# Kernel tuning notes

Measured on AMD Instinct MI355X. Metric: run time of the kernel, lower is better.

Reference implementation:

```python
import jax, jax.numpy as jnp
import numpy as np

THRESHOLD = 0.7
STRIDE = 1
PADDING = 1


def setup_inputs() -> dict:
    key = jax.random.key(0)
    k1, k2 = jax.random.split(key)
    B, CIN, H, W = 32, 256, 56, 56
    COUT, K = 256, 3
    x = jax.random.normal(k1, (B, CIN, H, W), dtype=jnp.float32)
    # kaiming-uniform-ish init: U(-bound, bound), bound = sqrt(6/fan_in)
    fan_in = CIN * K * K
    bound = float(np.sqrt(6.0 / fan_in))
    weight = jax.random.uniform(k2, (COUT, CIN, K, K), dtype=jnp.float32,
                                minval=-bound, maxval=bound)
    alpha = jnp.ones((1,), dtype=jnp.float32)
    bias = jnp.zeros((COUT,), dtype=jnp.float32)
    return {"x": x, "weight": weight, "alpha": alpha, "bias": bias}


def _ternize_ste(w, threshold):
    delta = threshold * jnp.mean(jnp.abs(jax.lax.stop_gradient(w)))
    ternary = jnp.where(w > delta, 1.0,
                        jnp.where(w < -delta, -1.0, 0.0)).astype(w.dtype)
    # straight-through: value = ternary, gradient = identity w.r.t. w
    return ternary + (w - jax.lax.stop_gradient(w))


def reference(x, weight, alpha, bias):
    w_t = _ternize_ste(weight, THRESHOLD) * alpha  # [COUT, CIN, K, K]
    out = jax.lax.conv_general_dilated(
        x, w_t,
        window_strides=(STRIDE, STRIDE),
        padding=[(PADDING, PADDING), (PADDING, PADDING)],
        dimension_numbers=("NCHW", "OIHW", "NCHW"),
    )
    return out + bias[None, :, None, None]
```

## Files before the change

### kernel.cpp

```cpp
#include <hip/hip_runtime.h>

typedef unsigned short ushort_t;
typedef short short8 __attribute__((ext_vector_type(8)));
typedef unsigned short ushort8 __attribute__((ext_vector_type(8)));
typedef float floatx4 __attribute__((ext_vector_type(4)));

#define N_W 589824

static __device__ __forceinline__ unsigned short f2bf(float f) {
    unsigned int u = __float_as_uint(f);
    u = (u + 0x7FFFu + ((u >> 16) & 1u)) >> 16;
    return (unsigned short)u;
}

static __device__ __forceinline__ void g2l16(const void* g, void* lds_base_uniform) {
    __builtin_amdgcn_global_load_lds(
        (__attribute__((address_space(1))) void*)g,
        (__attribute__((address_space(3))) void*)lds_base_uniform,
        16, 0, 0);
}

__global__ void absmean_kernel(const float* __restrict__ w, double* __restrict__ dsum) {
    int tid = blockIdx.x * blockDim.x + threadIdx.x;
    int stride = gridDim.x * blockDim.x;
    float local = 0.f;
    for (int i = tid; i < N_W; i += stride) local += fabsf(w[i]);
    for (int off = 32; off > 0; off >>= 1)
        local += __shfl_down(local, off, 64);
    __shared__ float part[4];
    int lane = threadIdx.x & 63, wv = threadIdx.x >> 6;
    if (lane == 0) part[wv] = local;
    __syncthreads();
    if (threadIdx.x == 0) {
        float s = part[0] + part[1] + part[2] + part[3];
        atomicAdd(dsum, (double)s);
    }
}

__global__ void ternarize_frag_kernel(const float* __restrict__ w, const double* __restrict__ dsum,
                                      ushort_t* __restrict__ wtf) {
    int o = blockIdx.x * 256 + threadIdx.x;
    float delta = 0.7f * (float)(*dsum / (double)N_W);
    int e   = o & 7;
    int l   = (o >> 3) & 15;
    int q   = (o >> 7) & 3;
    int i   = (o >> 9) & 3;
    int g   = (o >> 11) & 3;
    int t13 = o >> 13;
    int r9  = t13 % 9;
    int cb  = t13 / 9;
    int co  = g * 64 + i * 16 + l;
    int cin = cb * 32 + q * 8 + e;
    float v = w[(co * 256 + cin) * 9 + r9];
    float t = (v > delta) ? 1.f : ((v < -delta) ? -1.f : 0.f);
    wtf[o] = f2bf(t);
}

__global__ void ternarize_kernel(const float* __restrict__ w, const double* __restrict__ dsum,
                                 ushort_t* __restrict__ wt) {
    int o = blockIdx.x * 256 + threadIdx.x;
    float delta = 0.7f * (float)(*dsum / (double)N_W);
    int cin = o & 255;
    int co  = (o >> 8) & 255;
    int r   = o >> 16;
    float v = w[(co * 256 + cin) * 9 + r];
    float t = (v > delta) ? 1.f : ((v < -delta) ? -1.f : 0.f);
    wt[o] = f2bf(t);
}

__global__ void border_zero_kernel(ushort_t* __restrict__ xp) {
    int e = blockIdx.x * 256 + threadIdx.x;
    int cg   = e & 31;
    int rest = e >> 5;
    int pid  = rest % 228;
    int b    = rest / 228;
    int hh, ww;
    if (pid < 58)       { hh = 0;  ww = pid; }
    else if (pid < 116) { hh = 57; ww = pid - 58; }
    else {
        int p = pid - 116;
        hh = 1 + (p >> 1);
        ww = (p & 1) ? 57 : 0;
    }
    ushort8 z = (ushort8){0,0,0,0,0,0,0,0};
    *(ushort8*)&xp[(((b * 58 + hh) * 58 + ww) << 8) + cg * 8] = z;
}

__global__ __launch_bounds__(256)
void xcvt_kernel(const float* __restrict__ x, ushort_t* __restrict__ xp) {
    __shared__ float tile[64][65];
    const int px0 = blockIdx.x * 64;
    const int ci0 = blockIdx.y * 64;
    const int b   = blockIdx.z;
    const int row  = threadIdx.x >> 6;
    const int lane = threadIdx.x & 63;
#pragma unroll
    for (int k = 0; k < 16; ++k) {
        int ci_l = row * 16 + k;
        tile[ci_l][lane] = x[(b * 256 + ci0 + ci_l) * 3136 + px0 + lane];
    }
    __syncthreads();
#pragma unroll
    for (int p = 0; p < 2; ++p) {
        int c    = threadIdx.x + p * 256;
        int px_l = c >> 3;
        int cg   = c & 7;
        int px = px0 + px_l;
        int h = px / 56, w = px - h * 56;
        ushort8 v;
#pragma unroll
        for (int j = 0; j < 8; ++j) v[j] = f2bf(tile[cg * 8 + j][px_l]);
        *(ushort8*)&xp[(((b * 58 + h + 1) * 58 + (w + 1)) << 8) + ci0 + cg * 8] = v;
    }
}

__global__ __launch_bounds__(256, 3)
void conv_mfma4_kernel(const ushort_t* __restrict__ xp, const ushort_t* __restrict__ wtf,
                       const float* __restrict__ alpha, const float* __restrict__ bias,
                       float* __restrict__ out) {
    __shared__ __align__(16) ushort_t lds_x[2 * 512 * 8];

    const int tid  = threadIdx.x;
    const int b    = blockIdx.y;
    const int th   = blockIdx.x / 7;
    const int tw   = blockIdx.x - th * 7;
    const int h0   = th * 8;
    const int w0   = tw * 8;

    const int lane = tid & 63;
    const int wave = tid >> 6;
    const int l15  = lane & 15;
    const int quad = lane >> 4;
    const int hs   = l15 >> 3;
    const int ws   = l15 & 7;

    unsigned goff[2], loff[2];
#pragma unroll
    for (int t = 0; t < 2; ++t) {
        int s  = tid + t * 256;
        int ss = (s < 400) ? s : 399;
        int hr  = ss / 40;
        int rem = ss - hr * 40;
        int wc  = rem >> 2, cig = rem & 3;
        int gh = h0 + hr;
        int gw = w0 + wc;
        goff[t] = (unsigned)(((((b * 58 + gh) * 58 + gw) << 8) + (cig << 3)) * 2);
        loff[t] = (unsigned)((s & ~63) * 16);
    }
    const char* xpb = (const char*)xp;

    floatx4 acc[4][4];
#pragma unroll
    for (int i = 0; i < 4; ++i)
#pragma unroll
        for (int j = 0; j < 4; ++j)
            acc[i][j] = (floatx4){0.f, 0.f, 0.f, 0.f};

    const int gsel = wave;
    const ushort_t* wbase = wtf + gsel * 2048 + lane * 8;

    short8 af[3][4];
#pragma unroll
    for (int r = 0; r < 3; ++r)
#pragma unroll
        for (int i = 0; i < 4; ++i)
            af[r][i] = *(const short8*)(wbase + r * 8192 + i * 512);

#pragma unroll
    for (int t = 0; t < 2; ++t)
        g2l16(xpb + goff[t], (char*)lds_x + loff[t]);

    const int baseB = (hs * 10 + ws) * 32 + quad * 8;

    int cur = 0;
    for (int cb = 0; cb < 8; ++cb) {
        const ushort_t* wcb = wbase + cb * 73728;
        const ushort_t* wnx = wbase + ((cb < 7) ? cb + 1 : cb) * 73728;

        __syncthreads();

        if (cb < 7) {
#pragma unroll
            for (int t = 0; t < 2; ++t)
                g2l16(xpb + goff[t] + (cb + 1) * 64, (char*)lds_x + loff[t] + (cur ^ 1) * 8192);
        }

        const ushort_t* xb = lds_x + cur * 4096;

        short8 bfv[2][4];
#pragma unroll
        for (int j = 0; j < 4; ++j)
            bfv[0][j] = *(const short8*)&xb[baseB + (j * 2) * 320];

#pragma unroll
        for (int r9 = 0; r9 < 9; ++r9) {
            if (r9 < 8) {
                const int kh1 = (r9 + 1) / 3;
                const int kw1 = (r9 + 1) - kh1 * 3;
#pragma unroll
                for (int j = 0; j < 4; ++j)
                    bfv[(r9 + 1) & 1][j] =
                        *(const short8*)&xb[baseB + ((j * 2 + kh1) * 10 + kw1) * 32];
            }
            __builtin_amdgcn_s_setprio(1);
#pragma unroll
            for (int i = 0; i < 4; ++i)
#pragma unroll
                for (int j = 0; j < 4; ++j)
                    acc[i][j] = __builtin_amdgcn_mfma_f32_16x16x32_bf16(
                        af[r9 % 3][i], bfv[r9 & 1][j], acc[i][j], 0, 0, 0);
            __builtin_amdgcn_s_setprio(0);
            {
                const ushort_t* asrc = (r9 < 6) ? (wcb + (r9 + 3) * 8192)
                                                : (wnx + (r9 - 6) * 8192);
#pragma unroll
                for (int i = 0; i < 4; ++i)
                    af[r9 % 3][i] = *(const short8*)(asrc + i * 512);
            }
        }
        cur ^= 1;
    }

    const float a0 = alpha[0];
#pragma unroll
    for (int i = 0; i < 4; ++i) {
        int cob = gsel * 64 + i * 16 + quad * 4;
#pragma unroll
        for (int j = 0; j < 4; ++j) {
            int hh = h0 + j * 2 + hs;
            int ww = w0 + ws;
#pragma unroll
            for (int r = 0; r < 4; ++r) {
                int cog = cob + r;
                out[((b * 256 + cog) * 56 + hh) * 56 + ww] = acc[i][j][r] * a0 + bias[cog];
            }
        }
    }
}

__global__ __launch_bounds__(256, 2)
void conv_mfma_fallback_kernel(const float* __restrict__ x, const ushort_t* __restrict__ wt,
                               const float* __restrict__ alpha, const float* __restrict__ bias,
                               float* __restrict__ out) {
    __shared__ __align__(16) ushort_t lds_x[10 * 18 * 40];
    __shared__ __align__(16) ushort_t lds_a[128 * 40];
    const int tid  = threadIdx.x;
    const int b    = blockIdx.y;
    const int th   = blockIdx.x >> 2;
    const int tw   = blockIdx.x & 3;
    const int h0   = th * 8;
    const int w0   = tw * 16;
    const int co0  = blockIdx.z * 128;
    const int lane = tid & 63;
    const int wave = tid >> 6;
    const int l15  = lane & 15;
    const int quad = lane >> 4;
    const int wco  = (wave & 1) * 64;
    const int wrow = (wave >> 1) * 4;
    floatx4 acc[4][4];
#pragma unroll
    for (int i = 0; i < 4; ++i)
#pragma unroll
        for (int j = 0; j < 4; ++j)
            acc[i][j] = (floatx4){0.f, 0.f, 0.f, 0.f};
    const int co_l = tid >> 1;
    const int half = tid & 1;
    for (int cin0 = 0; cin0 < 256; cin0 += 32) {
        for (int e = tid; e < 5760; e += 256) {
            int hc = e % 18;
            int t2 = e / 18;
            int hr = t2 % 10;
            int ci = t2 / 10;
            int hh = h0 - 1 + hr;
            int ww = w0 - 1 + hc;
            float v = 0.f;
            if (hh >= 0 && hh < 56 && ww >= 0 && ww < 56)
                v = x[((b * 256 + cin0 + ci) * 3136) + hh * 56 + ww];
            lds_x[(hr * 18 + hc) * 40 + ci] = f2bf(v);
        }
        for (int r9 = 0; r9 < 9; ++r9) {
            {
                const short8* src = (const short8*)(wt + (((r9 * 256) + co0 + co_l) * 256 + cin0 + half * 16));
                short8 v0 = src[0];
                short8 v1 = src[1];
                *(short8*)&lds_a[co_l * 40 + half * 16]     = v0;
                *(short8*)&lds_a[co_l * 40 + half * 16 + 8] = v1;
            }
            __syncthreads();
            const int kh = r9 / 3;
            const int kw = r9 % 3;
            short8 af[4], bf[4];
#pragma unroll
            for (int j = 0; j < 4; ++j)
                bf[j] = *(const short8*)&lds_x[((wrow + j + kh) * 18 + (l15 + kw)) * 40 + quad * 8];
#pragma unroll
            for (int i = 0; i < 4; ++i)
                af[i] = *(const short8*)&lds_a[(wco + i * 16 + l15) * 40 + quad * 8];
#pragma unroll
            for (int i = 0; i < 4; ++i)
#pragma unroll
                for (int j = 0; j < 4; ++j)
                    acc[i][j] = __builtin_amdgcn_mfma_f32_16x16x32_bf16(af[i], bf[j], acc[i][j], 0, 0, 0);
            __syncthreads();
        }
    }
    const float a0 = alpha[0];
#pragma unroll
    for (int i = 0; i < 4; ++i) {
        int cob = co0 + wco + i * 16 + quad * 4;
#pragma unroll
        for (int j = 0; j < 4; ++j) {
            int hh = h0 + wrow + j;
            int ww = w0 + l15;
            if (ww < 56) {
#pragma unroll
                for (int r = 0; r < 4; ++r) {
                    int cog = cob + r;
                    out[((b * 256 + cog) * 56 + hh) * 56 + ww] = acc[i][j][r] * a0 + bias[cog];
                }
            }
        }
    }
}

extern "C" void kernel_launch(void* const* d_in, const int* in_sizes, int n_in,
                              void* d_out, int out_size, void* d_ws, size_t ws_size,
                              hipStream_t stream) {
    const float* x      = (const float*)d_in[0];
    const float* weight = (const float*)d_in[1];
    const float* alpha  = (const float*)d_in[2];
    const float* bias   = (const float*)d_in[3];
    float* out = (float*)d_out;

    double*   dsum = (double*)d_ws;
    ushort_t* wtf  = (ushort_t*)((char*)d_ws + 256);
    ushort_t* xp   = (ushort_t*)((char*)d_ws + 256 + 1179648);
    const size_t NEED = 256 + 1179648 + 55115776;

    hipMemsetAsync(d_ws, 0, 16, stream);
    absmean_kernel<<<256, 256, 0, stream>>>(weight, dsum);

    if (ws_size >= NEED) {
        ternarize_frag_kernel<<<N_W / 256, 256, 0, stream>>>(weight, dsum, wtf);
        border_zero_kernel<<<912, 256, 0, stream>>>(xp);
        dim3 cgrid(49, 4, 32);
        xcvt_kernel<<<cgrid, 256, 0, stream>>>(x, xp);
        dim3 grid(49, 32);
        conv_mfma4_kernel<<<grid, 256, 0, stream>>>(xp, wtf, alpha, bias, out);
    } else {
        ternarize_kernel<<<N_W / 256, 256, 0, stream>>>(weight, dsum, wtf);
        dim3 grid(28, 32, 2);
        conv_mfma_fallback_kernel<<<grid, 256, 0, stream>>>(x, wtf, alpha, bias, out);
    }
}
```

Baseline: 337.7 us.

## Store ternary weights as int8 bytes, expand to bf16 in-register; merge prep kernels

Ternary weights are now stored as one byte per element, holding the high byte of bf16 ±1/0, and expanded to bf16 with v_perm right before each MFMA. This halves the weight fragment traffic in the conv loop. The ternarize, border-zero and x-convert kernels are merged into a single prep launch that uses extra grid columns, which removes two launches. The block-level __syncthreads is replaced with an explicit waitcnt plus barrier, so the prefetched weight loads can stay in flight. The cost is some extra VALU perm work per r9 step and reliance on a hand-tuned vmcnt that has to match the number of outstanding loads.

```diff
diff --git a/kernel.cpp b/kernel.cpp
--- a/kernel.cpp
+++ b/kernel.cpp
@@ -1,9 +1,12 @@
 #include <hip/hip_runtime.h>
 
 typedef unsigned short ushort_t;
+typedef unsigned char uchar_t;
 typedef short short8 __attribute__((ext_vector_type(8)));
 typedef unsigned short ushort8 __attribute__((ext_vector_type(8)));
 typedef float floatx4 __attribute__((ext_vector_type(4)));
+typedef unsigned int uint2v __attribute__((ext_vector_type(2)));
+typedef unsigned int uint4v __attribute__((ext_vector_type(4)));
 
 #define N_W 589824
 
@@ -18,6 +21,15 @@
         (__attribute__((address_space(1))) void*)g,
         (__attribute__((address_space(3))) void*)lds_base_uniform,
         16, 0, 0);
+}
+
+static __device__ __forceinline__ short8 expand_tern(uint2v c) {
+    uint4v r;
+    r[0] = __builtin_amdgcn_perm(0x80808080u, c[0], 0x01040004u);
+    r[1] = __builtin_amdgcn_perm(0x80808080u, c[0], 0x03040204u);
+    r[2] = __builtin_amdgcn_perm(0x80808080u, c[1], 0x01040004u);
+    r[3] = __builtin_amdgcn_perm(0x80808080u, c[1], 0x03040204u);
+    return __builtin_bit_cast(short8, r);
 }
 
 __global__ void absmean_kernel(const float* __restrict__ w, double* __restrict__ dsum) {
@@ -37,23 +49,79 @@
     }
 }
 
-__global__ void ternarize_frag_kernel(const float* __restrict__ w, const double* __restrict__ dsum,
-                                      ushort_t* __restrict__ wtf) {
-    int o = blockIdx.x * 256 + threadIdx.x;
-    float delta = 0.7f * (float)(*dsum / (double)N_W);
-    int e   = o & 7;
-    int l   = (o >> 3) & 15;
-    int q   = (o >> 7) & 3;
-    int i   = (o >> 9) & 3;
-    int g   = (o >> 11) & 3;
-    int t13 = o >> 13;
-    int r9  = t13 % 9;
-    int cb  = t13 / 9;
-    int co  = g * 64 + i * 16 + l;
-    int cin = cb * 32 + q * 8 + e;
-    float v = w[(co * 256 + cin) * 9 + r9];
-    float t = (v > delta) ? 1.f : ((v < -delta) ? -1.f : 0.f);
-    wtf[o] = f2bf(t);
+__global__ __launch_bounds__(256)
+void prep_kernel(const float* __restrict__ x, const float* __restrict__ w,
+                 const double* __restrict__ dsum,
+                 uchar_t* __restrict__ wtf, ushort_t* __restrict__ xp) {
+    const int tid = threadIdx.x;
+
+    if (blockIdx.x == 50) {
+        const int id = blockIdx.y * 32 + blockIdx.z;
+        const float delta = 0.7f * (float)(*dsum / (double)N_W);
+        for (int k = tid; k < 4608; k += 256) {
+            int o = id * 4608 + k;
+            int e   = o & 7;
+            int l   = (o >> 3) & 15;
+            int q   = (o >> 7) & 3;
+            int i   = (o >> 9) & 3;
+            int g   = (o >> 11) & 3;
+            int t13 = o >> 13;
+            int r9  = t13 % 9;
+            int cb  = t13 / 9;
+            int co  = g * 64 + i * 16 + l;
+            int cin = cb * 32 + q * 8 + e;
+            float v = w[(co * 256 + cin) * 9 + r9];
+            wtf[o] = (v > delta) ? 0x3F : ((v < -delta) ? 0xBF : 0x00);
+        }
+        return;
+    }
+
+    if (blockIdx.x == 49) {
+        const int id = blockIdx.y * 32 + blockIdx.z;
+        ushort8 z = (ushort8){0,0,0,0,0,0,0,0};
+        for (int k = tid; k < 1824; k += 256) {
+            int e = id * 1824 + k;
+            int cg   = e & 31;
+            int rest = e >> 5;
+            int pid  = rest % 228;
+            int b    = rest / 228;
+            int hh, ww;
+            if (pid < 58)       { hh = 0;  ww = pid; }
+            else if (pid < 116) { hh = 57; ww = pid - 58; }
+            else {
+                int p = pid - 116;
+                hh = 1 + (p >> 1);
+                ww = (p & 1) ? 57 : 0;
+            }
+            *(ushort8*)&xp[(((b * 58 + hh) * 58 + ww) << 8) + cg * 8] = z;
+        }
+        return;
+    }
+
+    __shared__ float tile[64][65];
+    const int px0 = blockIdx.x * 64;
+    const int ci0 = blockIdx.y * 64;
+    const int b   = blockIdx.z;
+    const int row  = tid >> 6;
+    const int lane = tid & 63;
+#pragma unroll
+    for (int k = 0; k < 16; ++k) {
+        int ci_l = row * 16 + k;
+        tile[ci_l][lane] = x[(b * 256 + ci0 + ci_l) * 3136 + px0 + lane];
+    }
+    __syncthreads();
+#pragma unroll
+    for (int p = 0; p < 2; ++p) {
+        int c    = tid + p * 256;
+        int px_l = c >> 3;
+        int cg   = c & 7;
+        int px = px0 + px_l;
+        int h = px / 56, w2 = px - h * 56;
+        ushort8 v;
+#pragma unroll
+        for (int j = 0; j < 8; ++j) v[j] = f2bf(tile[cg * 8 + j][px_l]);
+        *(ushort8*)&xp[(((b * 58 + h + 1) * 58 + (w2 + 1)) << 8) + ci0 + cg * 8] = v;
+    }
 }
 
 __global__ void ternarize_kernel(const float* __restrict__ w, const double* __restrict__ dsum,
@@ -68,54 +136,8 @@
     wt[o] = f2bf(t);
 }
 
-__global__ void border_zero_kernel(ushort_t* __restrict__ xp) {
-    int e = blockIdx.x * 256 + threadIdx.x;
-    int cg   = e & 31;
-    int rest = e >> 5;
-    int pid  = rest % 228;
-    int b    = rest / 228;
-    int hh, ww;
-    if (pid < 58)       { hh = 0;  ww = pid; }
-    else if (pid < 116) { hh = 57; ww = pid - 58; }
-    else {
-        int p = pid - 116;
-        hh = 1 + (p >> 1);
-        ww = (p & 1) ? 57 : 0;
-    }
-    ushort8 z = (ushort8){0,0,0,0,0,0,0,0};
-    *(ushort8*)&xp[(((b * 58 + hh) * 58 + ww) << 8) + cg * 8] = z;
-}
-
-__global__ __launch_bounds__(256)
-void xcvt_kernel(const float* __restrict__ x, ushort_t* __restrict__ xp) {
-    __shared__ float tile[64][65];
-    const int px0 = blockIdx.x * 64;
-    const int ci0 = blockIdx.y * 64;
-    const int b   = blockIdx.z;
-    const int row  = threadIdx.x >> 6;
-    const int lane = threadIdx.x & 63;
-#pragma unroll
-    for (int k = 0; k < 16; ++k) {
-        int ci_l = row * 16 + k;
-        tile[ci_l][lane] = x[(b * 256 + ci0 + ci_l) * 3136 + px0 + lane];
-    }
-    __syncthreads();
-#pragma unroll
-    for (int p = 0; p < 2; ++p) {
-        int c    = threadIdx.x + p * 256;
-        int px_l = c >> 3;
-        int cg   = c & 7;
-        int px = px0 + px_l;
-        int h = px / 56, w = px - h * 56;
-        ushort8 v;
-#pragma unroll
-        for (int j = 0; j < 8; ++j) v[j] = f2bf(tile[cg * 8 + j][px_l]);
-        *(ushort8*)&xp[(((b * 58 + h + 1) * 58 + (w + 1)) << 8) + ci0 + cg * 8] = v;
-    }
-}
-
 __global__ __launch_bounds__(256, 3)
-void conv_mfma4_kernel(const ushort_t* __restrict__ xp, const ushort_t* __restrict__ wtf,
+void conv_mfma5_kernel(const ushort_t* __restrict__ xp, const uchar_t* __restrict__ wtf,
                        const float* __restrict__ alpha, const float* __restrict__ bias,
                        float* __restrict__ out) {
     __shared__ __align__(16) ushort_t lds_x[2 * 512 * 8];
@@ -157,33 +179,36 @@
             acc[i][j] = (floatx4){0.f, 0.f, 0.f, 0.f};
 
     const int gsel = wave;
-    const ushort_t* wbase = wtf + gsel * 2048 + lane * 8;
-
-    short8 af[3][4];
-#pragma unroll
-    for (int r = 0; r < 3; ++r)
-#pragma unroll
-        for (int i = 0; i < 4; ++i)
-            af[r][i] = *(const short8*)(wbase + r * 8192 + i * 512);
+    const uchar_t* wbase = wtf + gsel * 2048 + lane * 8;
 
 #pragma unroll
     for (int t = 0; t < 2; ++t)
         g2l16(xpb + goff[t], (char*)lds_x + loff[t]);
+    asm volatile("" ::: "memory");
+
+    uint2v afc[3][4];
+#pragma unroll
+    for (int r = 0; r < 3; ++r)
+#pragma unroll
+        for (int i = 0; i < 4; ++i)
+            afc[r][i] = *(const uint2v*)(wbase + r * 8192 + i * 512);
 
     const int baseB = (hs * 10 + ws) * 32 + quad * 8;
 
     int cur = 0;
     for (int cb = 0; cb < 8; ++cb) {
-        const ushort_t* wcb = wbase + cb * 73728;
-        const ushort_t* wnx = wbase + ((cb < 7) ? cb + 1 : cb) * 73728;
-
-        __syncthreads();
+        const uchar_t* wcb = wbase + cb * 73728;
+        const uchar_t* wnx = wbase + ((cb < 7) ? cb + 1 : cb) * 73728;
+
+        asm volatile("s_waitcnt vmcnt(12) lgkmcnt(0)" ::: "memory");
+        __builtin_amdgcn_s_barrier();
 
         if (cb < 7) {
 #pragma unroll
             for (int t = 0; t < 2; ++t)
                 g2l16(xpb + goff[t] + (cb + 1) * 64, (char*)lds_x + loff[t] + (cur ^ 1) * 8192);
         }
+        asm volatile("" ::: "memory");
 
         const ushort_t* xb = lds_x + cur * 4096;
 
@@ -202,20 +227,26 @@
                     bfv[(r9 + 1) & 1][j] =
                         *(const short8*)&xb[baseB + ((j * 2 + kh1) * 10 + kw1) * 32];
             }
+            short8 afx[4];
+#pragma unroll
+            for (int i = 0; i < 4; ++i)
+                afx[i] = expand_tern(afc[r9 % 3][i]);
+
             __builtin_amdgcn_s_setprio(1);
 #pragma unroll
             for (int i = 0; i < 4; ++i)
 #pragma unroll
                 for (int j = 0; j < 4; ++j)
                     acc[i][j] = __builtin_amdgcn_mfma_f32_16x16x32_bf16(
-                        af[r9 % 3][i], bfv[r9 & 1][j], acc[i][j], 0, 0, 0);
+                        afx[i], bfv[r9 & 1][j], acc[i][j], 0, 0, 0);
             __builtin_amdgcn_s_setprio(0);
+
             {
-                const ushort_t* asrc = (r9 < 6) ? (wcb + (r9 + 3) * 8192)
-                                                : (wnx + (r9 - 6) * 8192);
+                const uchar_t* asrc = (r9 < 6) ? (wcb + (r9 + 3) * 8192)
+                                               : (wnx + (r9 - 6) * 8192);
 #pragma unroll
                 for (int i = 0; i < 4; ++i)
-                    af[r9 % 3][i] = *(const short8*)(asrc + i * 512);
+                    afc[r9 % 3][i] = *(const uint2v*)(asrc + i * 512);
             }
         }
         cur ^= 1;
@@ -333,7 +364,8 @@
     float* out = (float*)d_out;
 
     double*   dsum = (double*)d_ws;
-    ushort_t* wtf  = (ushort_t*)((char*)d_ws + 256);
+    uchar_t*  wtf8 = (uchar_t*)((char*)d_ws + 256);
+    ushort_t* wt16 = (ushort_t*)((char*)d_ws + 256);
     ushort_t* xp   = (ushort_t*)((char*)d_ws + 256 + 1179648);
     const size_t NEED = 256 + 1179648 + 55115776;
 
@@ -341,15 +373,13 @@
     absmean_kernel<<<256, 256, 0, stream>>>(weight, dsum);
 
     if (ws_size >= NEED) {
-        ternarize_frag_kernel<<<N_W / 256, 256, 0, stream>>>(weight, dsum, wtf);
-        border_zero_kernel<<<912, 256, 0, stream>>>(xp);
-        dim3 cgrid(49, 4, 32);
-        xcvt_kernel<<<cgrid, 256, 0, stream>>>(x, xp);
+        dim3 pgrid(51, 4, 32);
+        prep_kernel<<<pgrid, 256, 0, stream>>>(x, weight, dsum, wtf8, xp);
         dim3 grid(49, 32);
-        conv_mfma4_kernel<<<grid, 256, 0, stream>>>(xp, wtf, alpha, bias, out);
+        conv_mfma5_kernel<<<grid, 256, 0, stream>>>(xp, wtf8, alpha, bias, out);
     } else {
-        ternarize_kernel<<<N_W / 256, 256, 0, stream>>>(weight, dsum, wtf);
+        ternarize_kernel<<<N_W / 256, 256, 0, stream>>>(weight, dsum, wt16);
         dim3 grid(28, 32, 2);
-        conv_mfma_fallback_kernel<<<grid, 256, 0, stream>>>(x, wtf, alpha, bias, out);
-    }
-}
+        conv_mfma_fallback_kernel<<<grid, 256, 0, stream>>>(x, wt16, alpha, bias, out);
+    }
+}
```

Result: faster. 318.0 us (-5.8%).
